# Kernel tuning notes

Hardware: AMD Instinct MI355X
Metric: run time of the kernel (lower is better)

## Reference

```python
import jax, jax.numpy as jnp
import numpy as np

B, NELEC, D, NION = 2048, 32, 128, 8
NSPIN = 2
NS = NELEC // NSPIN  # electrons (= orbitals) per spin


def setup_inputs() -> dict:
    key = jax.random.key(0)
    ks = jax.random.split(key, 6)
    eq_inputs = jax.random.normal(ks[0], (B, NELEC, D), dtype=jnp.float32)
    r_ei = jax.random.normal(ks[1], (B, NELEC, NION, 3), dtype=jnp.float32)
    W = jax.random.normal(ks[2], (NSPIN, D, NS), dtype=jnp.float32) / np.sqrt(D).astype(np.float32)
    b = jax.random.normal(ks[3], (NSPIN, NS), dtype=jnp.float32) * 0.1
    env_a = jax.random.normal(ks[4], (NSPIN, NION, NS), dtype=jnp.float32) * 0.5 + 1.0
    env_ion = jax.random.normal(ks[5], (NSPIN, NION, NS), dtype=jnp.float32) / np.sqrt(NION).astype(np.float32)
    return {"eq_inputs": eq_inputs, "r_ei": r_ei, "W": W, "b": b,
            "env_a": env_a, "env_ion": env_ion}


def _submatrix_row_indices(n):
    # idx[i, j] = row index kept at slot j after deleting row i
    j = np.arange(n - 1)
    idx = j[None, :] + (j[None, :] >= np.arange(n)[:, None])
    return jnp.asarray(idx)  # (n, n-1) int32


def reference(eq_inputs, r_ei, W, b, env_a, env_ion):
    # split into spins (equal split -> stack for vectorization)
    eq_s = jnp.stack(jnp.split(eq_inputs, NSPIN, axis=-2))   # (s,B,ns,d)
    rei_s = jnp.stack(jnp.split(r_ei, NSPIN, axis=-3))       # (s,B,ns,nion,3)

    # FermiNet orbital layer: linear part * isotropic exponential envelope
    linear = jnp.einsum("sbnd,sdo->sbno", eq_s, W) + b[:, None, None, :]
    dist = jnp.linalg.norm(rei_s, axis=-1)                   # (s,B,ns,nion)
    # exp(-||a (r - R)||) = exp(-|a| * ||r - R||) for isotropic scalar decay a
    exp_part = jnp.exp(-dist[..., None] * jnp.abs(env_a)[:, None, None, :, :])
    env = jnp.einsum("sbnio,sio->sbno", exp_part, env_ion)
    M = linear * env                                         # (s,B,ns,ns) square orbital matrices

    # slog cofactor antiequivariance along first column
    first = M[..., 0]                                        # (s,B,ns)
    osign = jnp.sign(first)
    olog = jnp.log(jnp.abs(first))
    y = M[..., 1:]                                           # delete column 0
    idx = _submatrix_row_indices(NS)
    sub = jnp.take(y, idx, axis=-2)                          # (s,B,ns,ns-1,ns-1): row i deleted
    csign, clog = jnp.linalg.slogdet(sub)                    # (s,B,ns)
    alt = jnp.asarray((-1.0) ** np.arange(NS), dtype=M.dtype)  # alternating signs (-1)^i
    a_sign = osign * csign * alt
    a_log = olog + clog

    # multiply equivariant inputs (slog form) by the per-particle antisymmetry
    out_sign = jnp.sign(eq_s) * a_sign[..., None]            # (s,B,ns,d)
    out_log = jnp.log(jnp.abs(eq_s)) + a_log[..., None]
    # stacked representation of the per-spin SLArrayList: (spin, {sign,log}, B, ns, d)
    return jnp.stack([out_sign, out_log], axis=1)
```

## Files before the change

### kernel.cpp

```cpp
#include <hip/hip_runtime.h>
#include <math.h>

#define NB 2048

__device__ __forceinline__ float signf_(float x) {
    return (x > 0.0f) ? 1.0f : ((x < 0.0f) ? -1.0f : 0.0f);
}

__global__ __launch_bounds__(256, 4)
void slogcof_kernel(const float* __restrict__ eq,
                    const float* __restrict__ rei,
                    const float* __restrict__ Wm,
                    const float* __restrict__ bias,
                    const float* __restrict__ env_a,
                    const float* __restrict__ env_ion,
                    float* __restrict__ out)
{
    __shared__ double sM[4][16][18];
    __shared__ double sDist[4][16][8];
    __shared__ float  sA[4][2][16];

    const int tid = threadIdx.x;
    const int w   = tid >> 6;
    const int l   = tid & 63;
    const int P   = blockIdx.x * 4 + w;
    const int s   = P >> 11;
    const int bb  = P & (NB - 1);

    const int o16 = l & 15;
    const int q4  = l >> 4;

    const float* eqp = eq + (size_t)bb * 4096 + s * 2048;

    #pragma unroll
    for (int rep = 0; rep < 2; ++rep) {
        const int n = (l >> 3) + rep * 8;
        const int i = l & 7;
        const float* rp = rei + (size_t)bb * 768 + s * 384 + n * 24 + i * 3;
        const double x = (double)rp[0], y = (double)rp[1], z = (double)rp[2];
        sDist[w][n][i] = sqrt(x * x + y * y + z * z);
    }
    __syncthreads();

    double accv[4] = {0.0, 0.0, 0.0, 0.0};
    {
        const float* Wp = Wm + s * 2048;
        const float* r0 = eqp + (4 * q4 + 0) * 128;
        const float* r1 = eqp + (4 * q4 + 1) * 128;
        const float* r2 = eqp + (4 * q4 + 2) * 128;
        const float* r3 = eqp + (4 * q4 + 3) * 128;
        #pragma unroll 4
        for (int d0 = 0; d0 < 128; d0 += 4) {
            const float4 a0 = *reinterpret_cast<const float4*>(r0 + d0);
            const float4 a1 = *reinterpret_cast<const float4*>(r1 + d0);
            const float4 a2 = *reinterpret_cast<const float4*>(r2 + d0);
            const float4 a3 = *reinterpret_cast<const float4*>(r3 + d0);
            const double w0 = (double)Wp[(d0 + 0) * 16 + o16];
            const double w1 = (double)Wp[(d0 + 1) * 16 + o16];
            const double w2 = (double)Wp[(d0 + 2) * 16 + o16];
            const double w3 = (double)Wp[(d0 + 3) * 16 + o16];
            accv[0] += (double)a0.x * w0 + (double)a0.y * w1 + (double)a0.z * w2 + (double)a0.w * w3;
            accv[1] += (double)a1.x * w0 + (double)a1.y * w1 + (double)a1.z * w2 + (double)a1.w * w3;
            accv[2] += (double)a2.x * w0 + (double)a2.y * w1 + (double)a2.z * w2 + (double)a2.w * w3;
            accv[3] += (double)a3.x * w0 + (double)a3.y * w1 + (double)a3.z * w2 + (double)a3.w * w3;
        }
    }

    {
        const double bd = (double)bias[s * 16 + o16];
        double ev[4] = {0.0, 0.0, 0.0, 0.0};
        #pragma unroll
        for (int i = 0; i < 8; ++i) {
            const double ea = fabs((double)env_a[s * 128 + i * 16 + o16]);
            const double ei = (double)env_ion[s * 128 + i * 16 + o16];
            #pragma unroll
            for (int j = 0; j < 4; ++j)
                ev[j] += exp(-sDist[w][4 * q4 + j][i] * ea) * ei;
        }
        #pragma unroll
        for (int j = 0; j < 4; ++j)
            sM[w][4 * q4 + j][o16] = (accv[j] + bd) * ev[j];
    }
    __syncthreads();

    {
        const int j = o16;
        double row[16];
        #pragma unroll
        for (int c = 0; c < 16; ++c) row[c] = sM[w][j][c];
        const double m0 = row[0];

        double logdet = 0.0;
        int dsign = 1;
        int used = 0;
        int mystep = -1;

        #pragma unroll
        for (int k = 0; k < 16; ++k) {
            unsigned key;
            {
                const float av = (float)fabs(row[k]);
                key = used ? (unsigned)j
                           : ((__float_as_uint(av) & 0xFFFFFFC0u) | 0x20u | (unsigned)j);
            }
            #pragma unroll
            for (int off = 8; off >= 1; off >>= 1) {
                const unsigned k2 = (unsigned)__shfl_xor((int)key, off, 16);
                if (k2 > key) key = k2;
            }
            const int p = (int)(key & 15u);
            const double pivv = __shfl(row[k], p, 16);
            logdet += (double)logf((float)fabs(pivv));
            if (pivv < 0.0) dsign = -dsign;
            else if (pivv == 0.0) dsign = 0;
            if (j == p) { used = 1; mystep = k; }
            const double minv = (pivv != 0.0) ? (1.0 / pivv) : 0.0;
            const double mul = row[k] * minv;
            const int upd = !used;
            #pragma unroll
            for (int c = k + 1; c < 16; ++c) {
                const double pv = __shfl(row[c], p, 16);
                if (upd) row[c] -= mul * pv;
            }
            if (upd) row[k] = mul;
        }

        int invc = 0;
        #pragma unroll
        for (int j2 = 0; j2 < 16; ++j2) {
            const int s2 = __shfl(mystep, j2, 16);
            if (j2 > j && mystep > s2) invc++;
        }
        #pragma unroll
        for (int off = 8; off >= 1; off >>= 1) invc += __shfl_xor(invc, off, 16);
        if (invc & 1) dsign = -dsign;

        double wv = 0.0;
        #pragma unroll
        for (int o = 0; o < 16; ++o) {
            double c0 = (mystep < o) ? (row[o] * wv) : 0.0;
            #pragma unroll
            for (int off = 8; off >= 1; off >>= 1) c0 += __shfl_xor(c0, off, 16);
            if (mystep == o) wv = (((o == 0) ? 1.0 : 0.0) - c0) / row[o];
        }
        double vv = 0.0;
        #pragma unroll
        for (int k = 15; k >= 0; --k) {
            double c0 = (mystep > k) ? (row[k] * vv) : 0.0;
            #pragma unroll
            for (int off = 8; off >= 1; off >>= 1) c0 += __shfl_xor(c0, off, 16);
            if (mystep == k) vv = wv - c0;
        }

        if (l < 16) {
            const double zj = vv;
            const float zs = (zj > 0.0) ? 1.0f : ((zj < 0.0) ? -1.0f : 0.0f);
            const float ms = (m0 > 0.0) ? 1.0f : ((m0 < 0.0) ? -1.0f : 0.0f);
            sA[w][0][j] = ms * (float)dsign * zs;
            sA[w][1][j] = logf((float)fabs(m0)) + (float)logdet + logf((float)fabs(zj));
        }
    }
    __syncthreads();

    float* op0 = out + (size_t)s * 8388608 + (size_t)bb * 2048;
    float* op1 = op0 + 4194304;
    #pragma unroll
    for (int it = 0; it < 8; ++it) {
        const int n  = it * 2 + (l >> 5);
        const int d0 = (l & 31) * 4;
        const float4 x = *reinterpret_cast<const float4*>(eqp + n * 128 + d0);
        const float a_s = sA[w][0][n];
        const float a_l = sA[w][1][n];
        float4 osg, olg;
        osg.x = signf_(x.x) * a_s;  olg.x = logf(fabsf(x.x)) + a_l;
        osg.y = signf_(x.y) * a_s;  olg.y = logf(fabsf(x.y)) + a_l;
        osg.z = signf_(x.z) * a_s;  olg.z = logf(fabsf(x.z)) + a_l;
        osg.w = signf_(x.w) * a_s;  olg.w = logf(fabsf(x.w)) + a_l;
        *reinterpret_cast<float4*>(op0 + n * 128 + d0) = osg;
        *reinterpret_cast<float4*>(op1 + n * 128 + d0) = olg;
    }
}

extern "C" void kernel_launch(void* const* d_in, const int* in_sizes, int n_in,
                              void* d_out, int out_size, void* d_ws, size_t ws_size,
                              hipStream_t stream) {
    (void)in_sizes; (void)n_in; (void)out_size; (void)d_ws; (void)ws_size;
    slogcof_kernel<<<dim3(1024), dim3(256), 0, stream>>>(
        (const float*)d_in[0],
        (const float*)d_in[1],
        (const float*)d_in[2],
        (const float*)d_in[3],
        (const float*)d_in[4],
        (const float*)d_in[5],
        (float*)d_out);
}
```

Before: 152.6 us.

## Use FP64 MFMA for orbital projection, custom exp, one wave per block

Replaces the scalar FP64 dot-product loop for the linear orbital layer with 16x16x4 FP64 MFMA instructions. The output layout is found by running an extra MFMA on index values, and the results are scattered through shared memory. The library exp in the envelope is replaced with a hand-written range-reduced polynomial exp. The launch also changes from 256-thread blocks holding four problems to 64-thread blocks holding one, which removes shared arrays indexed per wave. The MFMA lane mapping and the exp accuracy are correctness risks.

```diff
diff --git a/kernel.cpp b/kernel.cpp
--- a/kernel.cpp
+++ b/kernel.cpp
@@ -3,11 +3,35 @@
 
 #define NB 2048
 
+typedef double dbl4 __attribute__((ext_vector_type(4)));
+
 __device__ __forceinline__ float signf_(float x) {
     return (x > 0.0f) ? 1.0f : ((x < 0.0f) ? -1.0f : 0.0f);
 }
 
-__global__ __launch_bounds__(256, 4)
+__device__ __forceinline__ double fast_exp_neg(double y) {
+    const double LOG2E  = 1.4426950408889634074;
+    const double LN2_HI = 6.93147180369123816490e-01;
+    const double LN2_LO = 1.90821492927058770002e-10;
+    const double kd = __builtin_rint(y * LOG2E);
+    double r = __builtin_fma(-kd, LN2_HI, y);
+    r = __builtin_fma(-kd, LN2_LO, r);
+    double p = 2.755731922398589e-7;
+    p = __builtin_fma(p, r, 2.755731922398589e-6);
+    p = __builtin_fma(p, r, 2.480158730158730e-5);
+    p = __builtin_fma(p, r, 1.984126984126984e-4);
+    p = __builtin_fma(p, r, 1.388888888888889e-3);
+    p = __builtin_fma(p, r, 8.333333333333333e-3);
+    p = __builtin_fma(p, r, 4.166666666666667e-2);
+    p = __builtin_fma(p, r, 1.666666666666667e-1);
+    p = __builtin_fma(p, r, 0.5);
+    p = __builtin_fma(p, r, 1.0);
+    p = __builtin_fma(p, r, 1.0);
+    const long long ek = ((long long)(1023 + (int)kd)) << 52;
+    return p * __longlong_as_double(ek);
+}
+
+__global__ __launch_bounds__(64, 4)
 void slogcof_kernel(const float* __restrict__ eq,
                     const float* __restrict__ rei,
                     const float* __restrict__ Wm,
@@ -16,14 +40,12 @@
                     const float* __restrict__ env_ion,
                     float* __restrict__ out)
 {
-    __shared__ double sM[4][16][18];
-    __shared__ double sDist[4][16][8];
-    __shared__ float  sA[4][2][16];
-
-    const int tid = threadIdx.x;
-    const int w   = tid >> 6;
-    const int l   = tid & 63;
-    const int P   = blockIdx.x * 4 + w;
+    __shared__ double sM[16][18];
+    __shared__ double sDist[16][8];
+    __shared__ float  sA[2][16];
+
+    const int l   = threadIdx.x;
+    const int P   = blockIdx.x;
     const int s   = P >> 11;
     const int bb  = P & (NB - 1);
 
@@ -38,48 +60,62 @@
         const int i = l & 7;
         const float* rp = rei + (size_t)bb * 768 + s * 384 + n * 24 + i * 3;
         const double x = (double)rp[0], y = (double)rp[1], z = (double)rp[2];
-        sDist[w][n][i] = sqrt(x * x + y * y + z * z);
-    }
-    __syncthreads();
-
-    double accv[4] = {0.0, 0.0, 0.0, 0.0};
+        sDist[n][i] = sqrt(x * x + y * y + z * z);
+    }
+
+    double accv[4];
     {
         const float* Wp = Wm + s * 2048;
-        const float* r0 = eqp + (4 * q4 + 0) * 128;
-        const float* r1 = eqp + (4 * q4 + 1) * 128;
-        const float* r2 = eqp + (4 * q4 + 2) * 128;
-        const float* r3 = eqp + (4 * q4 + 3) * 128;
-        #pragma unroll 4
-        for (int d0 = 0; d0 < 128; d0 += 4) {
-            const float4 a0 = *reinterpret_cast<const float4*>(r0 + d0);
-            const float4 a1 = *reinterpret_cast<const float4*>(r1 + d0);
-            const float4 a2 = *reinterpret_cast<const float4*>(r2 + d0);
-            const float4 a3 = *reinterpret_cast<const float4*>(r3 + d0);
-            const double w0 = (double)Wp[(d0 + 0) * 16 + o16];
-            const double w1 = (double)Wp[(d0 + 1) * 16 + o16];
-            const double w2 = (double)Wp[(d0 + 2) * 16 + o16];
-            const double w3 = (double)Wp[(d0 + 3) * 16 + o16];
-            accv[0] += (double)a0.x * w0 + (double)a0.y * w1 + (double)a0.z * w2 + (double)a0.w * w3;
-            accv[1] += (double)a1.x * w0 + (double)a1.y * w1 + (double)a1.z * w2 + (double)a1.w * w3;
-            accv[2] += (double)a2.x * w0 + (double)a2.y * w1 + (double)a2.z * w2 + (double)a2.w * w3;
-            accv[3] += (double)a3.x * w0 + (double)a3.y * w1 + (double)a3.z * w2 + (double)a3.w * w3;
-        }
-    }
+        dbl4 acc0 = {0.0, 0.0, 0.0, 0.0};
+        dbl4 acc1 = {0.0, 0.0, 0.0, 0.0};
+        #pragma unroll 8
+        for (int i = 0; i < 32; i += 2) {
+            const double a0 = (double)eqp[o16 * 128 + 4 * i + q4];
+            const double b0 = (double)Wp[64 * i + l];
+            acc0 = __builtin_amdgcn_mfma_f64_16x16x4f64(a0, b0, acc0, 0, 0, 0);
+            const double a1 = (double)eqp[o16 * 128 + 4 * (i + 1) + q4];
+            const double b1 = (double)Wp[64 * (i + 1) + l];
+            acc1 = __builtin_amdgcn_mfma_f64_16x16x4f64(a1, b1, acc1, 0, 0, 0);
+        }
+        #pragma unroll
+        for (int r = 0; r < 4; ++r) accv[r] = acc0[r] + acc1[r];
+    }
+
+    int rowi[4], coli[4];
+    {
+        dbl4 pr = {0.0, 0.0, 0.0, 0.0};
+        dbl4 pc = {0.0, 0.0, 0.0, 0.0};
+        pr = __builtin_amdgcn_mfma_f64_16x16x4f64((double)o16, 1.0, pr, 0, 0, 0);
+        pc = __builtin_amdgcn_mfma_f64_16x16x4f64(1.0, (double)o16, pc, 0, 0, 0);
+        #pragma unroll
+        for (int r = 0; r < 4; ++r) {
+            rowi[r] = ((int)pr[r]) >> 2;
+            coli[r] = ((int)pc[r]) >> 2;
+        }
+    }
+
+    __syncthreads();
+
+    #pragma unroll
+    for (int r = 0; r < 4; ++r) sM[rowi[r]][coli[r]] = accv[r];
+    __syncthreads();
 
     {
         const double bd = (double)bias[s * 16 + o16];
-        double ev[4] = {0.0, 0.0, 0.0, 0.0};
+        double lin[4], ev[4] = {0.0, 0.0, 0.0, 0.0};
+        #pragma unroll
+        for (int jj = 0; jj < 4; ++jj) lin[jj] = sM[4 * q4 + jj][o16];
         #pragma unroll
         for (int i = 0; i < 8; ++i) {
             const double ea = fabs((double)env_a[s * 128 + i * 16 + o16]);
             const double ei = (double)env_ion[s * 128 + i * 16 + o16];
             #pragma unroll
-            for (int j = 0; j < 4; ++j)
-                ev[j] += exp(-sDist[w][4 * q4 + j][i] * ea) * ei;
-        }
-        #pragma unroll
-        for (int j = 0; j < 4; ++j)
-            sM[w][4 * q4 + j][o16] = (accv[j] + bd) * ev[j];
+            for (int jj = 0; jj < 4; ++jj)
+                ev[jj] += fast_exp_neg(-sDist[4 * q4 + jj][i] * ea) * ei;
+        }
+        #pragma unroll
+        for (int jj = 0; jj < 4; ++jj)
+            sM[4 * q4 + jj][o16] = (lin[jj] + bd) * ev[jj];
     }
     __syncthreads();
 
@@ -87,7 +123,7 @@
         const int j = o16;
         double row[16];
         #pragma unroll
-        for (int c = 0; c < 16; ++c) row[c] = sM[w][j][c];
+        for (int c = 0; c < 16; ++c) row[c] = sM[j][c];
         const double m0 = row[0];
 
         double logdet = 0.0;
@@ -156,8 +192,8 @@
             const double zj = vv;
             const float zs = (zj > 0.0) ? 1.0f : ((zj < 0.0) ? -1.0f : 0.0f);
             const float ms = (m0 > 0.0) ? 1.0f : ((m0 < 0.0) ? -1.0f : 0.0f);
-            sA[w][0][j] = ms * (float)dsign * zs;
-            sA[w][1][j] = logf((float)fabs(m0)) + (float)logdet + logf((float)fabs(zj));
+            sA[0][j] = ms * (float)dsign * zs;
+            sA[1][j] = logf((float)fabs(m0)) + (float)logdet + logf((float)fabs(zj));
         }
     }
     __syncthreads();
@@ -169,8 +205,8 @@
         const int n  = it * 2 + (l >> 5);
         const int d0 = (l & 31) * 4;
         const float4 x = *reinterpret_cast<const float4*>(eqp + n * 128 + d0);
-        const float a_s = sA[w][0][n];
-        const float a_l = sA[w][1][n];
+        const float a_s = sA[0][n];
+        const float a_l = sA[1][n];
         float4 osg, olg;
         osg.x = signf_(x.x) * a_s;  olg.x = logf(fabsf(x.x)) + a_l;
         osg.y = signf_(x.y) * a_s;  olg.y = logf(fabsf(x.y)) + a_l;
@@ -185,7 +221,7 @@
                               void* d_out, int out_size, void* d_ws, size_t ws_size,
                               hipStream_t stream) {
     (void)in_sizes; (void)n_in; (void)out_size; (void)d_ws; (void)ws_size;
-    slogcof_kernel<<<dim3(1024), dim3(256), 0, stream>>>(
+    slogcof_kernel<<<dim3(4096), dim3(64), 0, stream>>>(
         (const float*)d_in[0],
         (const float*)d_in[1],
         (const float*)d_in[2],
```

After: 136.1 us. 1.12x faster.
